# Performance work log

Measured on AMD Instinct MI355X. Metric: run time of the kernel, lower is better.

The kernel has to match this reference:

```python
import jax, jax.numpy as jnp
import numpy as np

B, L, D, H = 4, 2048, 1024, 16
HD = D // H


def setup_inputs() -> dict:
    key = jax.random.key(0)
    k0, k1, k2, k3, k4 = jax.random.split(key, 5)
    scale = 1.0 / np.sqrt(D)
    x = jax.random.normal(k0, (B, L, D), dtype=jnp.float32)
    Wk = jax.random.normal(k1, (D, D), dtype=jnp.float32) * scale
    Wv = jax.random.normal(k2, (D, D), dtype=jnp.float32) * scale
    Wr = jax.random.normal(k3, (D, D), dtype=jnp.float32) * scale
    Wo = jax.random.normal(k4, (D, D), dtype=jnp.float32) * scale
    # time_decay init: geometric decay per head, broadcast over head_dim
    decay = jnp.exp(-5.0 * jnp.arange(1, H + 1, dtype=jnp.float32) / H)
    time_decay = jnp.broadcast_to(decay[:, None], (H, HD)).astype(jnp.float32)
    time_first = jnp.full((H, HD), 0.5, dtype=jnp.float32)
    return {"x": x, "Wk": Wk, "Wv": Wv, "Wr": Wr, "Wo": Wo,
            "time_decay": time_decay, "time_first": time_first}


def reference(x, Wk, Wv, Wr, Wo, time_decay, time_first):
    b, l, d = x.shape
    h, hd = time_decay.shape
    # projections (nn.Linear: x @ W.T)
    k = (x @ Wk.T).reshape(b, l, h, hd)
    v = (x @ Wv.T).reshape(b, l, h, hd)
    r = jax.nn.sigmoid(x @ Wr.T).reshape(b, l, h, hd)

    decay = time_decay[None, :, :, None]   # (1,H,HD,1) broadcast over 'e' axis
    tf = time_first[None, :, :, None]      # (1,H,HD,1)

    def step(state, inp):
        k_t, v_t, r_t = inp                 # each (B,H,HD)
        # state: (B,H,HD,HD); outer product k_t (d) x v_t (e)
        state = state * decay + (k_t[..., :, None] * v_t[..., None, :]) * tf
        y_t = jnp.einsum('bhde,bhd->bhe', state, r_t)
        return state, y_t

    state0 = jnp.zeros((b, h, hd, hd), dtype=x.dtype)
    seq = (jnp.moveaxis(k, 1, 0), jnp.moveaxis(v, 1, 0), jnp.moveaxis(r, 1, 0))
    final_state, ys = jax.lax.scan(step, state0, seq)   # ys: (L,B,H,HD)
    y = jnp.moveaxis(ys, 0, 1).reshape(b, l, d) @ Wo.T
    return y, final_state
```

## Files before the change

### kernel.cpp

```cpp
#include <hip/hip_runtime.h>

typedef unsigned short u16;
typedef unsigned int   u32;
typedef __attribute__((ext_vector_type(8))) short bfrag;
typedef __attribute__((ext_vector_type(4))) float ffrag;

#define MFMA16(a,b,c) __builtin_amdgcn_mfma_f32_16x16x32_bf16((a),(b),(c),0,0,0)

#define GLL16(gp, lp) __builtin_amdgcn_global_load_lds( \
    (const __attribute__((address_space(1))) u32*)(gp), \
    (__attribute__((address_space(3))) u32*)(lp), 16, 0, 0)

__device__ __forceinline__ u16 f2b(float f) {
  u32 u = __float_as_uint(f);
  return (u16)((u + 0x7fffu + ((u >> 16) & 1u)) >> 16);
}
__device__ __forceinline__ float b2f(u16 v) { return __uint_as_float(((u32)v) << 16); }

__device__ __forceinline__ void unpack8(uint4 q, u16 e[8]) {
  e[0] = q.x & 0xffffu; e[1] = q.x >> 16;
  e[2] = q.y & 0xffffu; e[3] = q.y >> 16;
  e[4] = q.z & 0xffffu; e[5] = q.z >> 16;
  e[6] = q.w & 0xffffu; e[7] = q.w >> 16;
}

__global__ __launch_bounds__(256) void cvt_all(
    const float* __restrict__ x,  const float* __restrict__ wk,
    const float* __restrict__ wv, const float* __restrict__ wr,
    const float* __restrict__ wo,
    u16* __restrict__ xb, u16* __restrict__ wb, u16* __restrict__ wob)
{
  size_t i4 = ((size_t)blockIdx.x * 256 + threadIdx.x) * 4;
  const float* src; u16* dst; size_t off;
  if      (i4 <  8388608) { src = x;  dst = xb;            off = i4; }
  else if (i4 <  9437184) { src = wk; dst = wb;            off = i4 - 8388608; }
  else if (i4 < 10485760) { src = wv; dst = wb + 1048576;  off = i4 - 9437184; }
  else if (i4 < 11534336) { src = wr; dst = wb + 2097152;  off = i4 - 10485760; }
  else                    { src = wo; dst = wob;           off = i4 - 11534336; }
  float4 f = *(const float4*)(src + off);
  u16 o[4] = { f2b(f.x), f2b(f.y), f2b(f.z), f2b(f.w) };
  *(ushort4*)(dst + off) = make_ushort4(o[0], o[1], o[2], o[3]);
}

__global__ __launch_bounds__(256, 4) void k1_proj(
    const u16* __restrict__ xb, const u16* __restrict__ wb,
    const float* __restrict__ tf,
    u16* __restrict__ kws, u16* __restrict__ vws, u16* __restrict__ rws)
{
  __shared__ u16 As[2][128 * 32];
  __shared__ u16 Bs[2][128 * 32];
  const int tid  = threadIdx.x;
  const int wave = tid >> 6, lane = tid & 63;
  const int li = lane & 15, quad = lane >> 4;
  const int wm = (wave >> 1) * 64, wn = (wave & 1) * 64;

  const int bid = blockIdx.x;
  const int xcd = bid & 7, j = bid >> 3;
  const int m0 = ((xcd << 3) | (j & 7)) * 128;
  const int n0 = (j >> 3) * 128;

  ffrag acc[4][4];
#pragma unroll
  for (int i = 0; i < 4; ++i)
#pragma unroll
    for (int jj = 0; jj < 4; ++jj)
#pragma unroll
      for (int r = 0; r < 4; ++r) acc[i][jj][r] = 0.f;

  const int sr = lane >> 2, sc = (lane & 3) * 8;
  const u16* ga0 = xb + (size_t)(m0 + wave * 32 + sr) * 1024 + sc;
  const u16* gb0 = wb + (size_t)(n0 + wave * 32 + sr) * 1024 + sc;

#define STG(IT, BF) do { \
    const u16* ga_ = ga0 + (IT) * 32; \
    const u16* gb_ = gb0 + (IT) * 32; \
    GLL16(ga_,             As[BF] + wave * 1024); \
    GLL16(ga_ + 16 * 1024, As[BF] + wave * 1024 + 512); \
    GLL16(gb_,             Bs[BF] + wave * 1024); \
    GLL16(gb_ + 16 * 1024, Bs[BF] + wave * 1024 + 512); \
  } while (0)

  STG(0, 0);

  for (int it = 0; it < 32; ++it) {
    __syncthreads();
    if (it + 1 < 32) STG(it + 1, (it + 1) & 1);

    const int cb = it & 1;
    bfrag av[4], bv[4];
#pragma unroll
    for (int i = 0; i < 4; ++i)  av[i]  = *(const bfrag*)&As[cb][(wm + i * 16 + li) * 32 + quad * 8];
#pragma unroll
    for (int jj = 0; jj < 4; ++jj) bv[jj] = *(const bfrag*)&Bs[cb][(wn + jj * 16 + li) * 32 + quad * 8];
#pragma unroll
    for (int i = 0; i < 4; ++i)
#pragma unroll
      for (int jj = 0; jj < 4; ++jj)
        acc[i][jj] = MFMA16(av[i], bv[jj], acc[i][jj]);
  }
#undef STG

  const int sel = n0 >> 10;
#pragma unroll
  for (int i = 0; i < 4; ++i) {
#pragma unroll
    for (int jj = 0; jj < 4; ++jj) {
#pragma unroll
      for (int r = 0; r < 4; ++r) {
        int m = m0 + wm + i * 16 + quad * 4 + r;
        int n = n0 + wn + jj * 16 + li;
        int c = n & 1023;
        int bb = m >> 11, l = m & 2047;
        size_t dst = (size_t)((bb << 4) | (c >> 6)) * 131072 + (size_t)l * 64 + (c & 63);
        float v = acc[i][jj][r];
        if (sel == 0)      kws[dst] = f2b(v * tf[c]);
        else if (sel == 1) vws[dst] = f2b(v);
        else               rws[dst] = f2b(1.f / (1.f + __expf(-v)));
      }
    }
  }
}

#define ST 72

__global__ __launch_bounds__(256) void k2a_u(
    const u16* __restrict__ kws, const u16* __restrict__ vws,
    const float* __restrict__ td, u16* __restrict__ ut)
{
  __shared__ u16 KbarT[64 * ST];
  __shared__ u16 Vt[64 * ST];
  const int tid = threadIdx.x;
  const int lane = tid & 63, wave = tid >> 6;
  const int li = lane & 15, quad = lane >> 4;
  const int wr = (wave >> 1) * 32, wc = (wave & 1) * 32;
  const int bid = blockIdx.x;
  const int bh = bid >> 5, ch = bid & 31;
  const int h = bh & 15;
  const float l2D = log2f(td[h * 64]);
  const size_t base = (size_t)bh * 131072 + (size_t)ch * 4096;

#pragma unroll
  for (int it = 0; it < 2; ++it) {
    int c16 = tid + it * 256;
    int row = c16 >> 3, c8 = (c16 & 7) * 8;
    size_t g = base + (size_t)row * 64 + c8;
    uint4 kq = *(const uint4*)(kws + g);
    u16 ke[8]; unpack8(kq, ke);
    float sk = exp2f((float)(63 - row) * l2D);
#pragma unroll
    for (int jj = 0; jj < 8; ++jj) KbarT[(c8 + jj) * ST + row] = f2b(b2f(ke[jj]) * sk);
    uint4 vq = *(const uint4*)(vws + g);
    u16 ve[8]; unpack8(vq, ve);
#pragma unroll
    for (int jj = 0; jj < 8; ++jj) Vt[(c8 + jj) * ST + row] = ve[jj];
  }
  __syncthreads();

  ffrag U[2][2];
#pragma unroll
  for (int a = 0; a < 2; ++a)
#pragma unroll
    for (int b = 0; b < 2; ++b)
#pragma unroll
      for (int r = 0; r < 4; ++r) U[a][b][r] = 0.f;
#pragma unroll
  for (int kk = 0; kk < 64; kk += 32) {
    bfrag a0 = *(const bfrag*)&Vt[(wr + li) * ST + kk + quad * 8];
    bfrag a1 = *(const bfrag*)&Vt[(wr + 16 + li) * ST + kk + quad * 8];
    bfrag b0 = *(const bfrag*)&KbarT[(wc + li) * ST + kk + quad * 8];
    bfrag b1 = *(const bfrag*)&KbarT[(wc + 16 + li) * ST + kk + quad * 8];
    U[0][0] = MFMA16(a0, b0, U[0][0]);
    U[0][1] = MFMA16(a0, b1, U[0][1]);
    U[1][0] = MFMA16(a1, b0, U[1][0]);
    U[1][1] = MFMA16(a1, b1, U[1][1]);
  }

  u16* dst = ut + ((size_t)bid << 12);
#pragma unroll
  for (int ti = 0; ti < 2; ++ti)
#pragma unroll
    for (int tj = 0; tj < 2; ++tj)
#pragma unroll
      for (int r = 0; r < 4; ++r) {
        int e = wr + ti * 16 + quad * 4 + r;
        int d = wc + tj * 16 + li;
        dst[e * 64 + d] = f2b(U[ti][tj][r]);
      }
}

__global__ __launch_bounds__(256) void k2b_scan(
    const u16* __restrict__ ut, const float* __restrict__ td,
    u16* __restrict__ sbf, float* __restrict__ fstate)
{
  __shared__ float Sl[4 * 65];
  const int tid = threadIdx.x;
  const int bid = blockIdx.x;
  const int bh = bid >> 4, q = bid & 15;
  const int ed = q * 256 + tid;
  const int h = bh & 15;
  const float Dh = td[h * 64];
  const float DhC = exp2f(64.f * log2f(Dh));

  float S = 0.f;
  size_t idx = ((size_t)bh * 32) * 4096 + ed;
  for (int c = 0; c < 32; ++c, idx += 4096) {
    sbf[idx] = f2b(S);
    S = S * DhC + b2f(ut[idx]);
  }
  Sl[(tid >> 6) * 65 + (tid & 63)] = S;
  __syncthreads();
  int d = tid >> 2, el = tid & 3;
  fstate[(size_t)bh * 4096 + (size_t)d * 64 + q * 4 + el] = Sl[el * 65 + d];
}

__global__ __launch_bounds__(256) void k2c_y(
    const u16* __restrict__ kws, const u16* __restrict__ vws, const u16* __restrict__ rws,
    const u16* __restrict__ sbf, const float* __restrict__ td,
    u16* __restrict__ yws)
{
  __shared__ u16 Rc[64 * ST];
  __shared__ u16 KcA[64 * ST];
  __shared__ u16 Vt[64 * ST];
  __shared__ u16 STc[64 * ST];
  __shared__ float Dpow[65];

  const int tid = threadIdx.x;
  const int lane = tid & 63, wave = tid >> 6;
  const int li = lane & 15, quad = lane >> 4;
  const int wr = (wave >> 1) * 32, wc = (wave & 1) * 32;
  const int bid = blockIdx.x;
  const int bh = bid >> 5, ch = bid & 31;
  const int h = bh & 15, bb = bh >> 4;
  const float l2D = log2f(td[h * 64]);
  if (tid <= 64) Dpow[tid] = exp2f((float)tid * l2D);

  const size_t base = (size_t)bh * 131072 + (size_t)ch * 4096;
  const u16* sp = sbf + ((size_t)bid << 12);

#pragma unroll
  for (int it = 0; it < 2; ++it) {
    int c16 = tid + it * 256;
    int row = c16 >> 3, c8 = (c16 & 7) * 8;
    size_t g = base + (size_t)row * 64 + c8;
    *(uint4*)&Rc[row * ST + c8]  = *(const uint4*)(rws + g);
    *(uint4*)&KcA[row * ST + c8] = *(const uint4*)(kws + g);
    *(uint4*)&STc[row * ST + c8] = *(const uint4*)(sp + (size_t)row * 64 + c8);
    uint4 vq = *(const uint4*)(vws + g);
    u16 ve[8]; unpack8(vq, ve);
#pragma unroll
    for (int jj = 0; jj < 8; ++jj) Vt[(c8 + jj) * ST + row] = ve[jj];
  }
  __syncthreads();

  ffrag P[2][2], Y[2][2];
#pragma unroll
  for (int a = 0; a < 2; ++a)
#pragma unroll
    for (int b = 0; b < 2; ++b)
#pragma unroll
      for (int r = 0; r < 4; ++r) { P[a][b][r] = 0.f; Y[a][b][r] = 0.f; }

#pragma unroll
  for (int kk = 0; kk < 64; kk += 32) {
    bfrag a0 = *(const bfrag*)&Rc[(wr + li) * ST + kk + quad * 8];
    bfrag a1 = *(const bfrag*)&Rc[(wr + 16 + li) * ST + kk + quad * 8];
    bfrag b0 = *(const bfrag*)&KcA[(wc + li) * ST + kk + quad * 8];
    bfrag b1 = *(const bfrag*)&KcA[(wc + 16 + li) * ST + kk + quad * 8];
    P[0][0] = MFMA16(a0, b0, P[0][0]);
    P[0][1] = MFMA16(a0, b1, P[0][1]);
    P[1][0] = MFMA16(a1, b0, P[1][0]);
    P[1][1] = MFMA16(a1, b1, P[1][1]);
    bfrag s0 = *(const bfrag*)&STc[(wc + li) * ST + kk + quad * 8];
    bfrag s1 = *(const bfrag*)&STc[(wc + 16 + li) * ST + kk + quad * 8];
    Y[0][0] = MFMA16(a0, s0, Y[0][0]);
    Y[0][1] = MFMA16(a0, s1, Y[0][1]);
    Y[1][0] = MFMA16(a1, s0, Y[1][0]);
    Y[1][1] = MFMA16(a1, s1, Y[1][1]);
  }

#pragma unroll
  for (int ti = 0; ti < 2; ++ti)
#pragma unroll
    for (int tj = 0; tj < 2; ++tj)
#pragma unroll
      for (int r = 0; r < 4; ++r) {
        int t = wr + ti * 16 + quad * 4 + r;
        Y[ti][tj][r] *= Dpow[t + 1];
      }
  __syncthreads();

#pragma unroll
  for (int ti = 0; ti < 2; ++ti)
#pragma unroll
    for (int tj = 0; tj < 2; ++tj)
#pragma unroll
      for (int r = 0; r < 4; ++r) {
        int t = wr + ti * 16 + quad * 4 + r;
        int s = wc + tj * 16 + li;
        float v = (t >= s) ? P[ti][tj][r] * Dpow[t - s] : 0.f;
        KcA[t * ST + s] = f2b(v);
      }
  __syncthreads();

#pragma unroll
  for (int kk = 0; kk < 64; kk += 32) {
    bfrag aa0 = *(const bfrag*)&KcA[(wr + li) * ST + kk + quad * 8];
    bfrag aa1 = *(const bfrag*)&KcA[(wr + 16 + li) * ST + kk + quad * 8];
    bfrag vb0 = *(const bfrag*)&Vt[(wc + li) * ST + kk + quad * 8];
    bfrag vb1 = *(const bfrag*)&Vt[(wc + 16 + li) * ST + kk + quad * 8];
    Y[0][0] = MFMA16(aa0, vb0, Y[0][0]);
    Y[0][1] = MFMA16(aa0, vb1, Y[0][1]);
    Y[1][0] = MFMA16(aa1, vb0, Y[1][0]);
    Y[1][1] = MFMA16(aa1, vb1, Y[1][1]);
  }

#pragma unroll
  for (int ti = 0; ti < 2; ++ti)
#pragma unroll
    for (int tj = 0; tj < 2; ++tj)
#pragma unroll
      for (int r = 0; r < 4; ++r) {
        int t = wr + ti * 16 + quad * 4 + r;
        int e = wc + tj * 16 + li;
        yws[((size_t)(bb * 2048 + ch * 64 + t)) * 1024 + h * 64 + e] = f2b(Y[ti][tj][r]);
      }
}

__global__ __launch_bounds__(256, 4) void k3_out(
    const u16* __restrict__ yb, const u16* __restrict__ wob, float* __restrict__ out)
{
  __shared__ u16 As[2][128 * 32];
  __shared__ u16 Bs[2][128 * 32];
  const int tid  = threadIdx.x;
  const int wave = tid >> 6, lane = tid & 63;
  const int li = lane & 15, quad = lane >> 4;
  const int wm = (wave >> 1) * 64, wn = (wave & 1) * 64;

  const int bid = blockIdx.x;
  const int xcd = bid & 7, j = bid >> 3;
  const int m0 = ((xcd << 3) | (j & 7)) * 128;
  const int n0 = (j >> 3) * 128;

  ffrag acc[4][4];
#pragma unroll
  for (int i = 0; i < 4; ++i)
#pragma unroll
    for (int jj = 0; jj < 4; ++jj)
#pragma unroll
      for (int r = 0; r < 4; ++r) acc[i][jj][r] = 0.f;

  const int sr = lane >> 2, sc = (lane & 3) * 8;
  const u16* ga0 = yb  + (size_t)(m0 + wave * 32 + sr) * 1024 + sc;
  const u16* gb0 = wob + (size_t)(n0 + wave * 32 + sr) * 1024 + sc;

#define STG(IT, BF) do { \
    const u16* ga_ = ga0 + (IT) * 32; \
    const u16* gb_ = gb0 + (IT) * 32; \
    GLL16(ga_,             As[BF] + wave * 1024); \
    GLL16(ga_ + 16 * 1024, As[BF] + wave * 1024 + 512); \
    GLL16(gb_,             Bs[BF] + wave * 1024); \
    GLL16(gb_ + 16 * 1024, Bs[BF] + wave * 1024 + 512); \
  } while (0)

  STG(0, 0);

  for (int it = 0; it < 32; ++it) {
    __syncthreads();
    if (it + 1 < 32) STG(it + 1, (it + 1) & 1);

    const int cb = it & 1;
    bfrag av[4], bv[4];
#pragma unroll
    for (int i = 0; i < 4; ++i)  av[i]  = *(const bfrag*)&As[cb][(wm + i * 16 + li) * 32 + quad * 8];
#pragma unroll
    for (int jj = 0; jj < 4; ++jj) bv[jj] = *(const bfrag*)&Bs[cb][(wn + jj * 16 + li) * 32 + quad * 8];
#pragma unroll
    for (int i = 0; i < 4; ++i)
#pragma unroll
      for (int jj = 0; jj < 4; ++jj)
        acc[i][jj] = MFMA16(av[i], bv[jj], acc[i][jj]);
  }
#undef STG

#pragma unroll
  for (int i = 0; i < 4; ++i)
#pragma unroll
    for (int jj = 0; jj < 4; ++jj)
#pragma unroll
      for (int r = 0; r < 4; ++r) {
        int m = m0 + wm + i * 16 + quad * 4 + r;
        int n = n0 + wn + jj * 16 + li;
        out[(size_t)m * 1024 + n] = acc[i][jj][r];
      }
}

extern "C" void kernel_launch(void* const* d_in, const int* in_sizes, int n_in,
                              void* d_out, int out_size, void* d_ws, size_t ws_size,
                              hipStream_t stream) {
  const float* x  = (const float*)d_in[0];
  const float* Wk = (const float*)d_in[1];
  const float* Wv = (const float*)d_in[2];
  const float* Wr = (const float*)d_in[3];
  const float* Wo = (const float*)d_in[4];
  const float* td = (const float*)d_in[5];
  const float* tf = (const float*)d_in[6];
  float* out = (float*)d_out;

  u16* ws  = (u16*)d_ws;
  u16* xb  = ws;
  u16* wb  = ws + 8388608;
  u16* wob = ws + 11534336;
  u16* kws = ws + 12582912;
  u16* vws = ws + 20971520;
  u16* rws = ws + 29360128;
  u16* ut  = ws + 37748736;
  u16* sbf = ws + 54525952;
  u16* yws = xb;

  hipLaunchKernelGGL(cvt_all, dim3(12288), dim3(256), 0, stream,
                     x, Wk, Wv, Wr, Wo, xb, wb, wob);
  hipLaunchKernelGGL(k1_proj, dim3(1536), dim3(256), 0, stream,
                     xb, wb, tf, kws, vws, rws);
  hipLaunchKernelGGL(k2a_u, dim3(2048), dim3(256), 0, stream,
                     kws, vws, td, ut);
  hipLaunchKernelGGL(k2b_scan, dim3(1024), dim3(256), 0, stream,
                     ut, td, sbf, out + 8388608);
  hipLaunchKernelGGL(k2c_y, dim3(2048), dim3(256), 0, stream,
                     kws, vws, rws, sbf, td, yws);
  hipLaunchKernelGGL(k3_out, dim3(512), dim3(256), 0, stream,
                     yws, wob, out);
}
```

Baseline: 230.0 us.

## Process two chunks per block in chunk kernels and halve k3_out N tile

k2a_u and k2c_y now handle two consecutive 64-step chunks per block. All global loads for both chunks are issued up front into registers, so the second chunk's memory latency overlaps the first chunk's compute, and the grid is halved. k3_out moves to 128-thread blocks computing a 128x64 tile, which doubles the block count to 1024 for better CU occupancy. The cost is higher register pressure from the prefetched chunks and less reuse of A in the output GEMM.

```diff
diff --git a/kernel.cpp b/kernel.cpp
--- a/kernel.cpp
+++ b/kernel.cpp
@@ -134,58 +134,72 @@
   const int li = lane & 15, quad = lane >> 4;
   const int wr = (wave >> 1) * 32, wc = (wave & 1) * 32;
   const int bid = blockIdx.x;
-  const int bh = bid >> 5, ch = bid & 31;
+  const int bh = bid >> 4, cp = bid & 15;
   const int h = bh & 15;
   const float l2D = log2f(td[h * 64]);
-  const size_t base = (size_t)bh * 131072 + (size_t)ch * 4096;
-
+  const size_t base = (size_t)bh * 131072 + (size_t)(cp * 2) * 4096;
+
+  int rw[2], cc[2]; float sk[2];
+  uint4 kq[2][2], vq[2][2];
 #pragma unroll
   for (int it = 0; it < 2; ++it) {
     int c16 = tid + it * 256;
-    int row = c16 >> 3, c8 = (c16 & 7) * 8;
-    size_t g = base + (size_t)row * 64 + c8;
-    uint4 kq = *(const uint4*)(kws + g);
-    u16 ke[8]; unpack8(kq, ke);
-    float sk = exp2f((float)(63 - row) * l2D);
-#pragma unroll
-    for (int jj = 0; jj < 8; ++jj) KbarT[(c8 + jj) * ST + row] = f2b(b2f(ke[jj]) * sk);
-    uint4 vq = *(const uint4*)(vws + g);
-    u16 ve[8]; unpack8(vq, ve);
-#pragma unroll
-    for (int jj = 0; jj < 8; ++jj) Vt[(c8 + jj) * ST + row] = ve[jj];
-  }
-  __syncthreads();
-
-  ffrag U[2][2];
-#pragma unroll
-  for (int a = 0; a < 2; ++a)
-#pragma unroll
-    for (int b = 0; b < 2; ++b)
-#pragma unroll
-      for (int r = 0; r < 4; ++r) U[a][b][r] = 0.f;
-#pragma unroll
-  for (int kk = 0; kk < 64; kk += 32) {
-    bfrag a0 = *(const bfrag*)&Vt[(wr + li) * ST + kk + quad * 8];
-    bfrag a1 = *(const bfrag*)&Vt[(wr + 16 + li) * ST + kk + quad * 8];
-    bfrag b0 = *(const bfrag*)&KbarT[(wc + li) * ST + kk + quad * 8];
-    bfrag b1 = *(const bfrag*)&KbarT[(wc + 16 + li) * ST + kk + quad * 8];
-    U[0][0] = MFMA16(a0, b0, U[0][0]);
-    U[0][1] = MFMA16(a0, b1, U[0][1]);
-    U[1][0] = MFMA16(a1, b0, U[1][0]);
-    U[1][1] = MFMA16(a1, b1, U[1][1]);
-  }
-
-  u16* dst = ut + ((size_t)bid << 12);
-#pragma unroll
-  for (int ti = 0; ti < 2; ++ti)
-#pragma unroll
-    for (int tj = 0; tj < 2; ++tj)
-#pragma unroll
-      for (int r = 0; r < 4; ++r) {
-        int e = wr + ti * 16 + quad * 4 + r;
-        int d = wc + tj * 16 + li;
-        dst[e * 64 + d] = f2b(U[ti][tj][r]);
-      }
+    rw[it] = c16 >> 3; cc[it] = (c16 & 7) * 8;
+    sk[it] = exp2f((float)(63 - rw[it]) * l2D);
+    size_t g = base + (size_t)rw[it] * 64 + cc[it];
+    kq[0][it] = *(const uint4*)(kws + g);
+    vq[0][it] = *(const uint4*)(vws + g);
+    kq[1][it] = *(const uint4*)(kws + g + 4096);
+    vq[1][it] = *(const uint4*)(vws + g + 4096);
+  }
+
+#pragma unroll
+  for (int c = 0; c < 2; ++c) {
+#pragma unroll
+    for (int it = 0; it < 2; ++it) {
+      u16 ke[8]; unpack8(kq[c][it], ke);
+#pragma unroll
+      for (int jj = 0; jj < 8; ++jj)
+        KbarT[(cc[it] + jj) * ST + rw[it]] = f2b(b2f(ke[jj]) * sk[it]);
+      u16 ve[8]; unpack8(vq[c][it], ve);
+#pragma unroll
+      for (int jj = 0; jj < 8; ++jj)
+        Vt[(cc[it] + jj) * ST + rw[it]] = ve[jj];
+    }
+    __syncthreads();
+
+    ffrag U[2][2];
+#pragma unroll
+    for (int a = 0; a < 2; ++a)
+#pragma unroll
+      for (int b = 0; b < 2; ++b)
+#pragma unroll
+        for (int r = 0; r < 4; ++r) U[a][b][r] = 0.f;
+#pragma unroll
+    for (int kk = 0; kk < 64; kk += 32) {
+      bfrag a0 = *(const bfrag*)&Vt[(wr + li) * ST + kk + quad * 8];
+      bfrag a1 = *(const bfrag*)&Vt[(wr + 16 + li) * ST + kk + quad * 8];
+      bfrag b0 = *(const bfrag*)&KbarT[(wc + li) * ST + kk + quad * 8];
+      bfrag b1 = *(const bfrag*)&KbarT[(wc + 16 + li) * ST + kk + quad * 8];
+      U[0][0] = MFMA16(a0, b0, U[0][0]);
+      U[0][1] = MFMA16(a0, b1, U[0][1]);
+      U[1][0] = MFMA16(a1, b0, U[1][0]);
+      U[1][1] = MFMA16(a1, b1, U[1][1]);
+    }
+
+    u16* dst = ut + ((size_t)(bh * 32 + cp * 2 + c) << 12);
+#pragma unroll
+    for (int ti = 0; ti < 2; ++ti)
+#pragma unroll
+      for (int tj = 0; tj < 2; ++tj)
+#pragma unroll
+        for (int r = 0; r < 4; ++r) {
+          int e = wr + ti * 16 + quad * 4 + r;
+          int d = wc + tj * 16 + li;
+          dst[e * 64 + d] = f2b(U[ti][tj][r]);
+        }
+    if (c == 0) __syncthreads();
+  }
 }
 
 __global__ __launch_bounds__(256) void k2b_scan(
@@ -229,117 +243,134 @@
   const int li = lane & 15, quad = lane >> 4;
   const int wr = (wave >> 1) * 32, wc = (wave & 1) * 32;
   const int bid = blockIdx.x;
-  const int bh = bid >> 5, ch = bid & 31;
+  const int bh = bid >> 4, cp = bid & 15;
   const int h = bh & 15, bb = bh >> 4;
   const float l2D = log2f(td[h * 64]);
   if (tid <= 64) Dpow[tid] = exp2f((float)tid * l2D);
 
-  const size_t base = (size_t)bh * 131072 + (size_t)ch * 4096;
-  const u16* sp = sbf + ((size_t)bid << 12);
-
+  const size_t base = (size_t)bh * 131072 + (size_t)(cp * 2) * 4096;
+  const u16* sp0 = sbf + ((size_t)(bh * 32 + cp * 2) << 12);
+
+  int rw[2], cc[2];
+  uint4 rq[2][2], kq[2][2], sq[2][2], vq[2][2];
 #pragma unroll
   for (int it = 0; it < 2; ++it) {
     int c16 = tid + it * 256;
-    int row = c16 >> 3, c8 = (c16 & 7) * 8;
-    size_t g = base + (size_t)row * 64 + c8;
-    *(uint4*)&Rc[row * ST + c8]  = *(const uint4*)(rws + g);
-    *(uint4*)&KcA[row * ST + c8] = *(const uint4*)(kws + g);
-    *(uint4*)&STc[row * ST + c8] = *(const uint4*)(sp + (size_t)row * 64 + c8);
-    uint4 vq = *(const uint4*)(vws + g);
-    u16 ve[8]; unpack8(vq, ve);
-#pragma unroll
-    for (int jj = 0; jj < 8; ++jj) Vt[(c8 + jj) * ST + row] = ve[jj];
-  }
-  __syncthreads();
-
-  ffrag P[2][2], Y[2][2];
-#pragma unroll
-  for (int a = 0; a < 2; ++a)
-#pragma unroll
-    for (int b = 0; b < 2; ++b)
-#pragma unroll
-      for (int r = 0; r < 4; ++r) { P[a][b][r] = 0.f; Y[a][b][r] = 0.f; }
-
-#pragma unroll
-  for (int kk = 0; kk < 64; kk += 32) {
-    bfrag a0 = *(const bfrag*)&Rc[(wr + li) * ST + kk + quad * 8];
-    bfrag a1 = *(const bfrag*)&Rc[(wr + 16 + li) * ST + kk + quad * 8];
-    bfrag b0 = *(const bfrag*)&KcA[(wc + li) * ST + kk + quad * 8];
-    bfrag b1 = *(const bfrag*)&KcA[(wc + 16 + li) * ST + kk + quad * 8];
-    P[0][0] = MFMA16(a0, b0, P[0][0]);
-    P[0][1] = MFMA16(a0, b1, P[0][1]);
-    P[1][0] = MFMA16(a1, b0, P[1][0]);
-    P[1][1] = MFMA16(a1, b1, P[1][1]);
-    bfrag s0 = *(const bfrag*)&STc[(wc + li) * ST + kk + quad * 8];
-    bfrag s1 = *(const bfrag*)&STc[(wc + 16 + li) * ST + kk + quad * 8];
-    Y[0][0] = MFMA16(a0, s0, Y[0][0]);
-    Y[0][1] = MFMA16(a0, s1, Y[0][1]);
-    Y[1][0] = MFMA16(a1, s0, Y[1][0]);
-    Y[1][1] = MFMA16(a1, s1, Y[1][1]);
-  }
-
-#pragma unroll
-  for (int ti = 0; ti < 2; ++ti)
-#pragma unroll
-    for (int tj = 0; tj < 2; ++tj)
-#pragma unroll
-      for (int r = 0; r < 4; ++r) {
-        int t = wr + ti * 16 + quad * 4 + r;
-        Y[ti][tj][r] *= Dpow[t + 1];
-      }
-  __syncthreads();
-
-#pragma unroll
-  for (int ti = 0; ti < 2; ++ti)
-#pragma unroll
-    for (int tj = 0; tj < 2; ++tj)
-#pragma unroll
-      for (int r = 0; r < 4; ++r) {
-        int t = wr + ti * 16 + quad * 4 + r;
-        int s = wc + tj * 16 + li;
-        float v = (t >= s) ? P[ti][tj][r] * Dpow[t - s] : 0.f;
-        KcA[t * ST + s] = f2b(v);
-      }
-  __syncthreads();
-
-#pragma unroll
-  for (int kk = 0; kk < 64; kk += 32) {
-    bfrag aa0 = *(const bfrag*)&KcA[(wr + li) * ST + kk + quad * 8];
-    bfrag aa1 = *(const bfrag*)&KcA[(wr + 16 + li) * ST + kk + quad * 8];
-    bfrag vb0 = *(const bfrag*)&Vt[(wc + li) * ST + kk + quad * 8];
-    bfrag vb1 = *(const bfrag*)&Vt[(wc + 16 + li) * ST + kk + quad * 8];
-    Y[0][0] = MFMA16(aa0, vb0, Y[0][0]);
-    Y[0][1] = MFMA16(aa0, vb1, Y[0][1]);
-    Y[1][0] = MFMA16(aa1, vb0, Y[1][0]);
-    Y[1][1] = MFMA16(aa1, vb1, Y[1][1]);
-  }
-
-#pragma unroll
-  for (int ti = 0; ti < 2; ++ti)
-#pragma unroll
-    for (int tj = 0; tj < 2; ++tj)
-#pragma unroll
-      for (int r = 0; r < 4; ++r) {
-        int t = wr + ti * 16 + quad * 4 + r;
-        int e = wc + tj * 16 + li;
-        yws[((size_t)(bb * 2048 + ch * 64 + t)) * 1024 + h * 64 + e] = f2b(Y[ti][tj][r]);
-      }
-}
-
-__global__ __launch_bounds__(256, 4) void k3_out(
+    rw[it] = c16 >> 3; cc[it] = (c16 & 7) * 8;
+    size_t o = (size_t)rw[it] * 64 + cc[it];
+#pragma unroll
+    for (int c = 0; c < 2; ++c) {
+      rq[c][it] = *(const uint4*)(rws + base + c * 4096 + o);
+      kq[c][it] = *(const uint4*)(kws + base + c * 4096 + o);
+      vq[c][it] = *(const uint4*)(vws + base + c * 4096 + o);
+      sq[c][it] = *(const uint4*)(sp0 + c * 4096 + o);
+    }
+  }
+
+#pragma unroll
+  for (int c = 0; c < 2; ++c) {
+#pragma unroll
+    for (int it = 0; it < 2; ++it) {
+      *(uint4*)&Rc[rw[it] * ST + cc[it]]  = rq[c][it];
+      *(uint4*)&KcA[rw[it] * ST + cc[it]] = kq[c][it];
+      *(uint4*)&STc[rw[it] * ST + cc[it]] = sq[c][it];
+      u16 ve[8]; unpack8(vq[c][it], ve);
+#pragma unroll
+      for (int jj = 0; jj < 8; ++jj) Vt[(cc[it] + jj) * ST + rw[it]] = ve[jj];
+    }
+    __syncthreads();
+
+    ffrag P[2][2], Y[2][2];
+#pragma unroll
+    for (int a = 0; a < 2; ++a)
+#pragma unroll
+      for (int b = 0; b < 2; ++b)
+#pragma unroll
+        for (int r = 0; r < 4; ++r) { P[a][b][r] = 0.f; Y[a][b][r] = 0.f; }
+
+#pragma unroll
+    for (int kk = 0; kk < 64; kk += 32) {
+      bfrag a0 = *(const bfrag*)&Rc[(wr + li) * ST + kk + quad * 8];
+      bfrag a1 = *(const bfrag*)&Rc[(wr + 16 + li) * ST + kk + quad * 8];
+      bfrag b0 = *(const bfrag*)&KcA[(wc + li) * ST + kk + quad * 8];
+      bfrag b1 = *(const bfrag*)&KcA[(wc + 16 + li) * ST + kk + quad * 8];
+      P[0][0] = MFMA16(a0, b0, P[0][0]);
+      P[0][1] = MFMA16(a0, b1, P[0][1]);
+      P[1][0] = MFMA16(a1, b0, P[1][0]);
+      P[1][1] = MFMA16(a1, b1, P[1][1]);
+      bfrag s0 = *(const bfrag*)&STc[(wc + li) * ST + kk + quad * 8];
+      bfrag s1 = *(const bfrag*)&STc[(wc + 16 + li) * ST + kk + quad * 8];
+      Y[0][0] = MFMA16(a0, s0, Y[0][0]);
+      Y[0][1] = MFMA16(a0, s1, Y[0][1]);
+      Y[1][0] = MFMA16(a1, s0, Y[1][0]);
+      Y[1][1] = MFMA16(a1, s1, Y[1][1]);
+    }
+
+#pragma unroll
+    for (int ti = 0; ti < 2; ++ti)
+#pragma unroll
+      for (int tj = 0; tj < 2; ++tj)
+#pragma unroll
+        for (int r = 0; r < 4; ++r) {
+          int t = wr + ti * 16 + quad * 4 + r;
+          Y[ti][tj][r] *= Dpow[t + 1];
+        }
+    __syncthreads();
+
+#pragma unroll
+    for (int ti = 0; ti < 2; ++ti)
+#pragma unroll
+      for (int tj = 0; tj < 2; ++tj)
+#pragma unroll
+        for (int r = 0; r < 4; ++r) {
+          int t = wr + ti * 16 + quad * 4 + r;
+          int s = wc + tj * 16 + li;
+          float v = (t >= s) ? P[ti][tj][r] * Dpow[t - s] : 0.f;
+          KcA[t * ST + s] = f2b(v);
+        }
+    __syncthreads();
+
+#pragma unroll
+    for (int kk = 0; kk < 64; kk += 32) {
+      bfrag aa0 = *(const bfrag*)&KcA[(wr + li) * ST + kk + quad * 8];
+      bfrag aa1 = *(const bfrag*)&KcA[(wr + 16 + li) * ST + kk + quad * 8];
+      bfrag vb0 = *(const bfrag*)&Vt[(wc + li) * ST + kk + quad * 8];
+      bfrag vb1 = *(const bfrag*)&Vt[(wc + 16 + li) * ST + kk + quad * 8];
+      Y[0][0] = MFMA16(aa0, vb0, Y[0][0]);
+      Y[0][1] = MFMA16(aa0, vb1, Y[0][1]);
+      Y[1][0] = MFMA16(aa1, vb0, Y[1][0]);
+      Y[1][1] = MFMA16(aa1, vb1, Y[1][1]);
+    }
+
+    const int ch = cp * 2 + c;
+#pragma unroll
+    for (int ti = 0; ti < 2; ++ti)
+#pragma unroll
+      for (int tj = 0; tj < 2; ++tj)
+#pragma unroll
+        for (int r = 0; r < 4; ++r) {
+          int t = wr + ti * 16 + quad * 4 + r;
+          int e = wc + tj * 16 + li;
+          yws[((size_t)(bb * 2048 + ch * 64 + t)) * 1024 + h * 64 + e] = f2b(Y[ti][tj][r]);
+        }
+    if (c == 0) __syncthreads();
+  }
+}
+
+__global__ __launch_bounds__(128, 4) void k3_out(
     const u16* __restrict__ yb, const u16* __restrict__ wob, float* __restrict__ out)
 {
   __shared__ u16 As[2][128 * 32];
-  __shared__ u16 Bs[2][128 * 32];
+  __shared__ u16 Bs[2][64 * 32];
   const int tid  = threadIdx.x;
   const int wave = tid >> 6, lane = tid & 63;
   const int li = lane & 15, quad = lane >> 4;
-  const int wm = (wave >> 1) * 64, wn = (wave & 1) * 64;
+  const int wm = wave * 64;
 
   const int bid = blockIdx.x;
   const int xcd = bid & 7, j = bid >> 3;
   const int m0 = ((xcd << 3) | (j & 7)) * 128;
-  const int n0 = (j >> 3) * 128;
+  const int n0 = (j >> 3) * 64;
 
   ffrag acc[4][4];
 #pragma unroll
@@ -350,16 +381,18 @@
       for (int r = 0; r < 4; ++r) acc[i][jj][r] = 0.f;
 
   const int sr = lane >> 2, sc = (lane & 3) * 8;
-  const u16* ga0 = yb  + (size_t)(m0 + wave * 32 + sr) * 1024 + sc;
+  const u16* ga0 = yb  + (size_t)(m0 + wave * 64 + sr) * 1024 + sc;
   const u16* gb0 = wob + (size_t)(n0 + wave * 32 + sr) * 1024 + sc;
 
 #define STG(IT, BF) do { \
     const u16* ga_ = ga0 + (IT) * 32; \
     const u16* gb_ = gb0 + (IT) * 32; \
-    GLL16(ga_,             As[BF] + wave * 1024); \
-    GLL16(ga_ + 16 * 1024, As[BF] + wave * 1024 + 512); \
-    GLL16(gb_,             Bs[BF] + wave * 1024); \
-    GLL16(gb_ + 16 * 1024, Bs[BF] + wave * 1024 + 512); \
+    GLL16(ga_,             As[BF] + (wave * 64 +  0) * 32); \
+    GLL16(ga_ + 16 * 1024, As[BF] + (wave * 64 + 16) * 32); \
+    GLL16(ga_ + 32 * 1024, As[BF] + (wave * 64 + 32) * 32); \
+    GLL16(ga_ + 48 * 1024, As[BF] + (wave * 64 + 48) * 32); \
+    GLL16(gb_,             Bs[BF] + (wave * 32 +  0) * 32); \
+    GLL16(gb_ + 16 * 1024, Bs[BF] + (wave * 32 + 16) * 32); \
   } while (0)
 
   STG(0, 0);
@@ -373,7 +406,7 @@
 #pragma unroll
     for (int i = 0; i < 4; ++i)  av[i]  = *(const bfrag*)&As[cb][(wm + i * 16 + li) * 32 + quad * 8];
 #pragma unroll
-    for (int jj = 0; jj < 4; ++jj) bv[jj] = *(const bfrag*)&Bs[cb][(wn + jj * 16 + li) * 32 + quad * 8];
+    for (int jj = 0; jj < 4; ++jj) bv[jj] = *(const bfrag*)&Bs[cb][(jj * 16 + li) * 32 + quad * 8];
 #pragma unroll
     for (int i = 0; i < 4; ++i)
 #pragma unroll
@@ -389,7 +422,7 @@
 #pragma unroll
       for (int r = 0; r < 4; ++r) {
         int m = m0 + wm + i * 16 + quad * 4 + r;
-        int n = n0 + wn + jj * 16 + li;
+        int n = n0 + jj * 16 + li;
         out[(size_t)m * 1024 + n] = acc[i][jj][r];
       }
 }
@@ -421,12 +454,12 @@
                      x, Wk, Wv, Wr, Wo, xb, wb, wob);
   hipLaunchKernelGGL(k1_proj, dim3(1536), dim3(256), 0, stream,
                      xb, wb, tf, kws, vws, rws);
-  hipLaunchKernelGGL(k2a_u, dim3(2048), dim3(256), 0, stream,
+  hipLaunchKernelGGL(k2a_u, dim3(1024), dim3(256), 0, stream,
                      kws, vws, td, ut);
   hipLaunchKernelGGL(k2b_scan, dim3(1024), dim3(256), 0, stream,
                      ut, td, sbf, out + 8388608);
-  hipLaunchKernelGGL(k2c_y, dim3(2048), dim3(256), 0, stream,
+  hipLaunchKernelGGL(k2c_y, dim3(1024), dim3(256), 0, stream,
                      kws, vws, rws, sbf, td, yws);
-  hipLaunchKernelGGL(k3_out, dim3(512), dim3(256), 0, stream,
+  hipLaunchKernelGGL(k3_out, dim3(1024), dim3(128), 0, stream,
                      yws, wob, out);
 }
```

New measurement: 254.5 us. 10.7% more time.

## Double K-tile depth in projection GEMM with XOR-swizzled LDS layout

Applied to the files above, without the earlier changes.

Raises the projection GEMM's K-step from 32 to 64, which halves the number of barrier-separated iterations and issues more MFMAs per sync. The LDS tile layout now uses an XOR swizzle on the column chunk to avoid bank conflicts on the wider 64-element rows. Shared memory per block doubles and the occupancy hint drops from 4 to 2 blocks per CU, so there is less latency hiding between blocks.

```diff
diff --git a/kernel.cpp b/kernel.cpp
--- a/kernel.cpp
+++ b/kernel.cpp
@@ -42,13 +42,13 @@
   *(ushort4*)(dst + off) = make_ushort4(o[0], o[1], o[2], o[3]);
 }
 
-__global__ __launch_bounds__(256, 4) void k1_proj(
+__global__ __launch_bounds__(256, 2) void k1_proj(
     const u16* __restrict__ xb, const u16* __restrict__ wb,
     const float* __restrict__ tf,
     u16* __restrict__ kws, u16* __restrict__ vws, u16* __restrict__ rws)
 {
-  __shared__ u16 As[2][128 * 32];
-  __shared__ u16 Bs[2][128 * 32];
+  __shared__ u16 As[2][128 * 64];
+  __shared__ u16 Bs[2][128 * 64];
   const int tid  = threadIdx.x;
   const int wave = tid >> 6, lane = tid & 63;
   const int li = lane & 15, quad = lane >> 4;
@@ -67,36 +67,55 @@
 #pragma unroll
       for (int r = 0; r < 4; ++r) acc[i][jj][r] = 0.f;
 
-  const int sr = lane >> 2, sc = (lane & 3) * 8;
-  const u16* ga0 = xb + (size_t)(m0 + wave * 32 + sr) * 1024 + sc;
-  const u16* gb0 = wb + (size_t)(n0 + wave * 32 + sr) * 1024 + sc;
+  const int s_row = lane >> 3;
+  const int s_col = ((lane & 7) * 8) ^ (((lane >> 3) & 7) << 3);
+  const u16* ga0 = xb + (size_t)(m0 + wave * 32 + s_row) * 1024 + s_col;
+  const u16* gb0 = wb + (size_t)(n0 + wave * 32 + s_row) * 1024 + s_col;
 
 #define STG(IT, BF) do { \
-    const u16* ga_ = ga0 + (IT) * 32; \
-    const u16* gb_ = gb0 + (IT) * 32; \
-    GLL16(ga_,             As[BF] + wave * 1024); \
-    GLL16(ga_ + 16 * 1024, As[BF] + wave * 1024 + 512); \
-    GLL16(gb_,             Bs[BF] + wave * 1024); \
-    GLL16(gb_ + 16 * 1024, Bs[BF] + wave * 1024 + 512); \
+    const u16* ga_ = ga0 + (IT) * 64; \
+    const u16* gb_ = gb0 + (IT) * 64; \
+    u16* la_ = As[BF] + (wave * 32) * 64; \
+    u16* lb_ = Bs[BF] + (wave * 32) * 64; \
+    GLL16(ga_,             la_); \
+    GLL16(ga_ +  8 * 1024, la_ +  8 * 64); \
+    GLL16(ga_ + 16 * 1024, la_ + 16 * 64); \
+    GLL16(ga_ + 24 * 1024, la_ + 24 * 64); \
+    GLL16(gb_,             lb_); \
+    GLL16(gb_ +  8 * 1024, lb_ +  8 * 64); \
+    GLL16(gb_ + 16 * 1024, lb_ + 16 * 64); \
+    GLL16(gb_ + 24 * 1024, lb_ + 24 * 64); \
   } while (0)
 
   STG(0, 0);
 
-  for (int it = 0; it < 32; ++it) {
+  const int c0 = (quad * 8) ^ ((li & 7) << 3);
+
+  for (int it = 0; it < 16; ++it) {
     __syncthreads();
-    if (it + 1 < 32) STG(it + 1, (it + 1) & 1);
+    if (it + 1 < 16) STG(it + 1, (it + 1) & 1);
 
     const int cb = it & 1;
-    bfrag av[4], bv[4];
-#pragma unroll
-    for (int i = 0; i < 4; ++i)  av[i]  = *(const bfrag*)&As[cb][(wm + i * 16 + li) * 32 + quad * 8];
-#pragma unroll
-    for (int jj = 0; jj < 4; ++jj) bv[jj] = *(const bfrag*)&Bs[cb][(wn + jj * 16 + li) * 32 + quad * 8];
-#pragma unroll
-    for (int i = 0; i < 4; ++i)
-#pragma unroll
-      for (int jj = 0; jj < 4; ++jj)
-        acc[i][jj] = MFMA16(av[i], bv[jj], acc[i][jj]);
+    bfrag av[4][2], bv[4][2];
+#pragma unroll
+    for (int i = 0; i < 4; ++i) {
+      int rb = (wm + i * 16 + li) * 64;
+      av[i][0] = *(const bfrag*)&As[cb][rb + c0];
+      av[i][1] = *(const bfrag*)&As[cb][rb + (c0 ^ 32)];
+    }
+#pragma unroll
+    for (int jj = 0; jj < 4; ++jj) {
+      int rb = (wn + jj * 16 + li) * 64;
+      bv[jj][0] = *(const bfrag*)&Bs[cb][rb + c0];
+      bv[jj][1] = *(const bfrag*)&Bs[cb][rb + (c0 ^ 32)];
+    }
+#pragma unroll
+    for (int kh = 0; kh < 2; ++kh)
+#pragma unroll
+      for (int i = 0; i < 4; ++i)
+#pragma unroll
+        for (int jj = 0; jj < 4; ++jj)
+          acc[i][jj] = MFMA16(av[i][kh], bv[jj][kh], acc[i][jj]);
   }
 #undef STG
 
```

Result: slower. 243.0 us (+5.7%).
